# Kernel optimization log

Hardware: AMD Instinct MI355X
Metric: run time of the kernel (lower is better)

The kernel has to match this reference:

```python
import jax, jax.numpy as jnp
import numpy as np

B, T, C = 2, 2048, 1024
HS, DS = 8, 32      # short heads, short qk dim
HL, DL = 8, 128     # long heads, long qk dim
HD = 64             # value/output head dim = n_embd // n_head
WIN_S, WIN_L = 256, 1024
NEG = jnp.finfo(jnp.float32).min


def _window_mask(t, window):
    # additive mask: disallow future (i<j) and tokens older than the window
    i = jnp.arange(t)[:, None]
    j = jnp.arange(t)[None, :]
    bad = (i - j < 0) | (i - j >= window)
    return bad.astype(jnp.float32) * NEG  # [T,T]


def _attn(x, Wqk, Wv, n_h, d_qk, d_v, window):
    b, t, _ = x.shape
    qk = x @ Wqk                                      # [B,T,2*n_h*d_qk]
    q, k = jnp.split(qk, 2, axis=-1)
    q = q.reshape(b, t, n_h, d_qk).transpose(0, 2, 1, 3)  # [B,H,T,dqk]
    k = k.reshape(b, t, n_h, d_qk).transpose(0, 2, 1, 3)
    v = (x @ Wv).reshape(b, t, n_h, d_v).transpose(0, 2, 1, 3)  # [B,H,T,dv]
    scale = 1.0 / jnp.sqrt(jnp.float32(d_qk))
    scores = jnp.einsum('bhqd,bhkd->bhqk', q, k) * scale
    scores = scores + _window_mask(t, window)
    p = jax.nn.softmax(scores, axis=-1)
    return jnp.einsum('bhqk,bhkd->bhqd', p, v)        # [B,H,T,dv]


def setup_inputs() -> dict:
    key = jax.random.key(0)
    ks = jax.random.split(key, 6)
    s = 0.02
    return {
        'x': jax.random.normal(ks[0], (B, T, C), dtype=jnp.float32),
        'Wqk_short': jax.random.normal(ks[1], (C, 2 * HS * DS), dtype=jnp.float32) * s,
        'Wv_short': jax.random.normal(ks[2], (C, HS * HD), dtype=jnp.float32) * s,
        'Wqk_long': jax.random.normal(ks[3], (C, 2 * HL * DL), dtype=jnp.float32) * s,
        'Wv_long': jax.random.normal(ks[4], (C, HL * HD), dtype=jnp.float32) * s,
        'Wproj': jax.random.normal(ks[5], (C, C), dtype=jnp.float32) * s,
    }


def reference(x, Wqk_short, Wv_short, Wqk_long, Wv_long, Wproj):
    b, t, c = x.shape
    y_short = _attn(x, Wqk_short, Wv_short, HS, DS, HD, WIN_S)  # [B,HS,T,HD]
    y_long = _attn(x, Wqk_long, Wv_long, HL, DL, HD, WIN_L)     # [B,HL,T,HD]
    y = jnp.concatenate([y_short, y_long], axis=1)              # [B,H,T,HD]
    y = y.transpose(0, 2, 1, 3).reshape(b, t, c)
    return y @ Wproj
```

## Files before the change

kernel.cpp:

```cpp
#include <hip/hip_runtime.h>
#include <math.h>

#define B_    2
#define T_    2048
#define C_    1024
#define HS_   8
#define DS_   32
#define HL_   8
#define DL_   128
#define HD_   64
#define WINS_ 256
#define WINL_ 1024
#define NALL_ 3584

typedef __bf16 bf16x8 __attribute__((ext_vector_type(8)));
typedef float floatx4 __attribute__((ext_vector_type(4)));

__device__ __forceinline__ ushort f2bf(float f) {
    union { float f; unsigned u; } v; v.f = f;
    unsigned r = v.u + 0x7fff + ((v.u >> 16) & 1);
    return (ushort)(r >> 16);
}
__device__ __forceinline__ float bf2f(ushort u) {
    union { unsigned u; float f; } v; v.u = ((unsigned)u) << 16;
    return v.f;
}

__device__ __forceinline__ float dpp_bfly(float x, int ctrl_unused) { return x; }
#define DPP_STEP(x, ctrl, op)                                                \
    {                                                                        \
        float _t = __builtin_bit_cast(                                       \
            float, __builtin_amdgcn_update_dpp(                              \
                       0, __builtin_bit_cast(int, (x)), (ctrl), 0xf, 0xf,    \
                       true));                                               \
        (x) = op((x), _t);                                                   \
    }
__device__ __forceinline__ float dpp_max16(float x) {
    DPP_STEP(x, 0xB1, fmaxf);
    DPP_STEP(x, 0x4E, fmaxf);
    DPP_STEP(x, 0x141, fmaxf);
    DPP_STEP(x, 0x140, fmaxf);
    return x;
}
__device__ __forceinline__ float dpp_add16(float x) {
#define FADD_(a, b) ((a) + (b))
    DPP_STEP(x, 0xB1, FADD_);
    DPP_STEP(x, 0x4E, FADD_);
    DPP_STEP(x, 0x141, FADD_);
    DPP_STEP(x, 0x140, FADD_);
#undef FADD_
    return x;
}

__device__ __forceinline__ void gload_lds16(const void* g, void* l) {
    __builtin_amdgcn_global_load_lds(
        (const __attribute__((address_space(1))) void*)g,
        (__attribute__((address_space(3))) void*)l, 16, 0, 0);
}

__global__ __launch_bounds__(256) void prep(
    const float* __restrict__ x, ushort* __restrict__ x16,
    const float* __restrict__ Wqk_s, const float* __restrict__ Wv_s,
    const float* __restrict__ Wqk_l, const float* __restrict__ Wv_l,
    const float* __restrict__ Wproj, ushort* __restrict__ WallT,
    ushort* __restrict__ WprojT) {
    __shared__ float t[32][33];
    int bid = blockIdx.x;
    if (bid < 4096) {
        const int i = bid * 256 + threadIdx.x;
        float4 v = ((const float4*)x)[i];
        ushort4 o;
        o.x = f2bf(v.x); o.y = f2bf(v.y); o.z = f2bf(v.z); o.w = f2bf(v.w);
        ((ushort4*)x16)[i] = o;
        return;
    }
    bid -= 4096;
    const float* W; ushort* WT; int N, rowoff;
    if (bid < 512)       { W = Wqk_s; WT = WallT;  N = 512;  rowoff = 0; }
    else if (bid < 1024) { bid -= 512;  W = Wv_s;  WT = WallT;  N = 512;  rowoff = 512; }
    else if (bid < 3072) { bid -= 1024; W = Wqk_l; WT = WallT;  N = 2048; rowoff = 1024; }
    else if (bid < 3584) { bid -= 3072; W = Wv_l;  WT = WallT;  N = 512;  rowoff = 3072; }
    else                 { bid -= 3584; W = Wproj; WT = WprojT; N = 1024; rowoff = 0; }
    const int nt = N / 32;
    const int n0 = (bid % nt) * 32;
    const int k0 = (bid / nt) * 32;
    const int tx = threadIdx.x & 31;
    const int ty = threadIdx.x >> 5;
#pragma unroll
    for (int i = 0; i < 4; ++i)
        t[ty + 8 * i][tx] = W[(size_t)(k0 + ty + 8 * i) * N + n0 + tx];
    __syncthreads();
#pragma unroll
    for (int i = 0; i < 4; ++i)
        WT[(size_t)(rowoff + n0 + ty + 8 * i) * 1024 + k0 + tx] =
            f2bf(t[tx][ty + 8 * i]);
}

template <int BM, typename OT>
__global__ __launch_bounds__(256) void gemm_bf16(const ushort* __restrict__ A,
                                                 const ushort* __restrict__ BT,
                                                 OT* __restrict__ Cm,
                                                 int M, int N, int K) {
    __shared__ ushort As[BM * 32];
    __shared__ ushort Bs[128 * 32];
    constexpr int NI = BM / 32;
    const int tid = threadIdx.x;
    const int m0 = blockIdx.y * BM;
    const int n0 = blockIdx.x * 128;
    const int wave = tid >> 6;
    const int lane = tid & 63;
    const int wm = (wave >> 1) * (BM / 2);
    const int wn = (wave & 1) * 64;
    const int l15 = lane & 15;
    const int quad = lane >> 4;

    const int srow = tid >> 2;
    const int sc = (tid & 3) * 8;

    floatx4 acc[NI][4] = {};

    const ushort* Ap0 = A + (size_t)(m0 + srow) * K + sc;
    const ushort* Ap1 = A + (size_t)(m0 + (srow & 63) + 64) * K + sc;
    const ushort* Bp0 = BT + (size_t)(n0 + srow) * K + sc;
    const ushort* Bp1 = BT + (size_t)(n0 + srow + 64) * K + sc;

    ushort* AsB0 = &As[wave * 512];
    ushort* AsB1 = &As[(wave * 512 + 2048) % (BM * 32)];
    ushort* BsB0 = &Bs[wave * 512];
    ushort* BsB1 = &Bs[wave * 512 + 2048];

    for (int kt = 0; kt < K; kt += 32) {
        __syncthreads();
        gload_lds16(Ap0 + kt, AsB0);
        if constexpr (BM == 128) gload_lds16(Ap1 + kt, AsB1);
        gload_lds16(Bp0 + kt, BsB0);
        gload_lds16(Bp1 + kt, BsB1);
        __syncthreads();

        bf16x8 af[NI], bfr[4];
#pragma unroll
        for (int i = 0; i < NI; ++i)
            af[i] = *(const bf16x8*)&As[(wm + i * 16 + l15) * 32 + quad * 8];
#pragma unroll
        for (int j = 0; j < 4; ++j)
            bfr[j] = *(const bf16x8*)&Bs[(wn + j * 16 + l15) * 32 + quad * 8];
#pragma unroll
        for (int i = 0; i < NI; ++i)
#pragma unroll
            for (int j = 0; j < 4; ++j)
                acc[i][j] = __builtin_amdgcn_mfma_f32_16x16x32_bf16(
                    af[i], bfr[j], acc[i][j], 0, 0, 0);
    }

#pragma unroll
    for (int i = 0; i < NI; ++i)
#pragma unroll
        for (int j = 0; j < 4; ++j)
#pragma unroll
            for (int r = 0; r < 4; ++r) {
                const size_t idx = (size_t)(m0 + wm + i * 16 + quad * 4 + r) * N +
                                   n0 + wn + j * 16 + l15;
                if constexpr (sizeof(OT) == 2)
                    Cm[idx] = f2bf(acc[i][j][r]);
                else
                    Cm[idx] = acc[i][j][r];
            }
}

__global__ __launch_bounds__(256) void vtrans(const ushort* __restrict__ act,
                                              ushort* __restrict__ vt) {
    __shared__ ushort tile[64][72];
    const int t0 = blockIdx.x * 64;
    const int gh = blockIdx.y;
    const int b = blockIdx.z;
    const int col = (gh < 8) ? (512 + gh * 64) : (3072 + (gh - 8) * 64);
    const ushort* src = act + (size_t)(b * T_ + t0) * NALL_ + col;
    {
        const int tr = threadIdx.x >> 2;
        const int ch = threadIdx.x & 3;
        *(int4*)&tile[tr][ch * 8] =
            *(const int4*)(src + (size_t)tr * NALL_ + ch * 8);
        *(int4*)&tile[tr][(ch + 4) * 8] =
            *(const int4*)(src + (size_t)tr * NALL_ + (ch + 4) * 8);
    }
    __syncthreads();
    const int d = threadIdx.x >> 2;
    const int ts = (threadIdx.x & 3) * 16;
    ushort tmp[16];
#pragma unroll
    for (int i = 0; i < 16; ++i) tmp[i] = tile[ts + i][d];
    ushort* dst = vt + ((size_t)(b * 16 + gh) * HD_ + d) * T_ + t0 + ts;
    *(int4*)dst = *(int4*)tmp;
    *(int4*)(dst + 8) = *(int4*)(tmp + 8);
}

template <int D, int WIN, bool SPLIT>
__device__ __forceinline__ void attn_dev(
    const ushort* __restrict__ act, const ushort* __restrict__ vt,
    ushort* __restrict__ y, ushort* __restrict__ po, float* __restrict__ pm,
    float* __restrict__ pl, float scale2, int qoff, int koff, int head_off,
    int h, int gh, int b, int t0, int zs, ushort* lds) {
    constexpr int STR = D + 8;
    constexpr int PSTR = 72;
    constexpr int NKS = D / 32;
    constexpr int QCH = D / 8;
    constexpr int NKLD = (64 * QCH) / 256;

    ushort* Ks = lds;
    ushort* VTs = Ks + 64 * STR;
    ushort* Ps = VTs + 64 * PSTR;

    const int tid = threadIdx.x;
    const int wave = tid >> 6;
    const int lane = tid & 63;
    const int l15 = lane & 15;
    const int quad = lane >> 4;
    const int qmin = t0 + wave * 16;

    int k0s = t0 - WIN + 1;
    if (k0s < 0) k0s = 0;
    k0s &= ~63;

    int ks_begin = k0s, ks_last = t0;
    if (SPLIT) {
        const int nt = ((t0 - k0s) >> 6) + 1;
        const int ntlo = (nt + 1) >> 1;
        if (zs == 0) {
            ks_last = k0s + (ntlo - 1) * 64;
        } else {
            if (ntlo >= nt) {
#pragma unroll
                for (int r = 0; r < 4; ++r) {
                    const int t = qmin + quad * 4 + r;
                    const size_t ridx =
                        (((size_t)(zs * 2 + b) * 8 + h) * T_ + t);
                    if (l15 == 0) { pm[ridx] = -1e30f; pl[ridx] = 0.f; }
#pragma unroll
                    for (int j = 0; j < 4; ++j)
                        po[ridx * 64 + j * 16 + l15] = 0;
                }
                return;
            }
            ks_begin = k0s + ntlo * 64;
        }
    }

    const ushort* qbase = act + (size_t)(b * T_ + t0) * NALL_ + qoff + h * D;
    const ushort* kbase = act + (size_t)(b * T_) * NALL_ + koff + h * D;
    const ushort* vtb = vt + (size_t)((b * 16 + gh) * HD_) * T_;

    int krow[NKLD], kch[NKLD];
#pragma unroll
    for (int i = 0; i < NKLD; ++i) {
        const int idx = tid + 256 * i;
        krow[i] = idx / QCH;
        kch[i] = idx % QCH;
    }
    const int vd0 = tid >> 3, vc0 = (tid & 7) * 8;
    const int vd1 = (tid + 256) >> 3, vc1 = ((tid + 256) & 7) * 8;

    int4 kreg[NKLD], vreg0, vreg1;
#pragma unroll
    for (int i = 0; i < NKLD; ++i)
        kreg[i] = *(const int4*)(kbase + (size_t)(ks_begin + krow[i]) * NALL_ +
                                 kch[i] * 8);
    vreg0 = *(const int4*)(vtb + (size_t)vd0 * T_ + ks_begin + vc0);
    vreg1 = *(const int4*)(vtb + (size_t)vd1 * T_ + ks_begin + vc1);

    for (int idx = tid; idx < 64 * QCH; idx += 256) {
        const int row = idx / QCH;
        const int ch = idx % QCH;
        *(int4*)&Ks[row * STR + ch * 8] =
            *(const int4*)(qbase + (size_t)row * NALL_ + ch * 8);
    }
    __syncthreads();
    bf16x8 qa[NKS];
#pragma unroll
    for (int ks = 0; ks < NKS; ++ks)
        qa[ks] = *(const bf16x8*)&Ks[(wave * 16 + l15) * STR + ks * 32 + quad * 8];

    float m_i[4], l_i[4];
    floatx4 o_acc[4] = {};
#pragma unroll
    for (int r = 0; r < 4; ++r) { m_i[r] = -1e30f; l_i[r] = 0.f; }

    for (int k0 = ks_begin; k0 <= ks_last; k0 += 64) {
        __syncthreads();
#pragma unroll
        for (int i = 0; i < NKLD; ++i)
            *(int4*)&Ks[krow[i] * STR + kch[i] * 8] = kreg[i];
        *(int4*)&VTs[vd0 * PSTR + vc0] = vreg0;
        *(int4*)&VTs[vd1 * PSTR + vc1] = vreg1;
        __syncthreads();
        if (k0 + 64 <= ks_last) {
#pragma unroll
            for (int i = 0; i < NKLD; ++i)
                kreg[i] = *(const int4*)(kbase +
                                         (size_t)(k0 + 64 + krow[i]) * NALL_ +
                                         kch[i] * 8);
            vreg0 = *(const int4*)(vtb + (size_t)vd0 * T_ + k0 + 64 + vc0);
            vreg1 = *(const int4*)(vtb + (size_t)vd1 * T_ + k0 + 64 + vc1);
        }

        floatx4 s[4] = {};
#pragma unroll
        for (int ks = 0; ks < NKS; ++ks) {
#pragma unroll
            for (int j = 0; j < 4; ++j) {
                const bf16x8 bb =
                    *(const bf16x8*)&Ks[(j * 16 + l15) * STR + ks * 32 + quad * 8];
                s[j] = __builtin_amdgcn_mfma_f32_16x16x32_bf16(qa[ks], bb, s[j],
                                                               0, 0, 0);
            }
        }

        const bool full = (k0 + 63 <= qmin) && ((qmin + 15) - k0 <= WIN - 1);
        if (full) {
#pragma unroll
            for (int j = 0; j < 4; ++j)
#pragma unroll
                for (int r = 0; r < 4; ++r) s[j][r] *= scale2;
        } else {
#pragma unroll
            for (int j = 0; j < 4; ++j) {
                const int kj = k0 + j * 16 + l15;
#pragma unroll
                for (int r = 0; r < 4; ++r) {
                    const int rel = (qmin + quad * 4 + r) - kj;
                    s[j][r] = (rel < 0 || rel >= WIN) ? -1e30f : s[j][r] * scale2;
                }
            }
        }

#pragma unroll
        for (int r = 0; r < 4; ++r) {
            float rm = fmaxf(fmaxf(s[0][r], s[1][r]), fmaxf(s[2][r], s[3][r]));
            rm = dpp_max16(rm);
            const float mn = fmaxf(m_i[r], rm);
            const float a = exp2f(m_i[r] - mn);
            m_i[r] = mn;
            float sum = 0.f;
#pragma unroll
            for (int j = 0; j < 4; ++j) {
                const float e = exp2f(s[j][r] - mn);
                sum += e;
                Ps[(wave * 16 + quad * 4 + r) * PSTR + j * 16 + l15] = f2bf(e);
            }
            sum = dpp_add16(sum);
            l_i[r] = l_i[r] * a + sum;
#pragma unroll
            for (int j = 0; j < 4; ++j) o_acc[j][r] *= a;
        }

#pragma unroll
        for (int kks = 0; kks < 2; ++kks) {
            const bf16x8 pa =
                *(const bf16x8*)&Ps[(wave * 16 + l15) * PSTR + kks * 32 + quad * 8];
#pragma unroll
            for (int j = 0; j < 4; ++j) {
                const bf16x8 vb =
                    *(const bf16x8*)&VTs[(j * 16 + l15) * PSTR + kks * 32 + quad * 8];
                o_acc[j] = __builtin_amdgcn_mfma_f32_16x16x32_bf16(pa, vb, o_acc[j],
                                                                   0, 0, 0);
            }
        }
    }

    if (SPLIT) {
#pragma unroll
        for (int r = 0; r < 4; ++r) {
            const int t = qmin + quad * 4 + r;
            const size_t ridx = (((size_t)(zs * 2 + b) * 8 + h) * T_ + t);
            if (l15 == 0) { pm[ridx] = m_i[r]; pl[ridx] = l_i[r]; }
#pragma unroll
            for (int j = 0; j < 4; ++j)
                po[ridx * 64 + j * 16 + l15] = f2bf(o_acc[j][r]);
        }
    } else {
#pragma unroll
        for (int r = 0; r < 4; ++r) {
            const float inv = 1.f / l_i[r];
            ushort* yrow = y + (size_t)(b * T_ + qmin + quad * 4 + r) * C_ +
                           head_off + h * HD_;
#pragma unroll
            for (int j = 0; j < 4; ++j)
                yrow[j * 16 + l15] = f2bf(o_acc[j][r] * inv);
        }
    }
}

__global__ __launch_bounds__(256, 4) void attn_sched(
    const ushort* __restrict__ act, const ushort* __restrict__ vt,
    ushort* __restrict__ y, ushort* __restrict__ po, float* __restrict__ pm,
    float* __restrict__ pl) {
    extern __shared__ ushort smem[];
    int x = blockIdx.x;
    if (x < 1024) {
        const int zs = x & 1;
        const int b = (x >> 1) & 1;
        const int h = (x >> 2) & 7;
        const int t0 = (31 - (x >> 5)) * 64;
        attn_dev<DL_, WINL_, true>(act, vt, y, po, pm, pl,
                                   0.12752021352994164f,
                                   1024, 2048, 512, h, 8 + h, b, t0, zs, smem);
    } else {
        x -= 1024;
        const int b = x & 1;
        const int h = (x >> 1) & 7;
        const int t0 = (31 - (x >> 4)) * 64;
        attn_dev<DS_, WINS_, false>(act, vt, y, po, pm, pl,
                                    0.2550404270598833f,
                                    0, 256, 0, h, h, b, t0, 0, smem);
    }
}

__global__ __launch_bounds__(256) void combine(const ushort* __restrict__ po,
                                               const float* __restrict__ pm,
                                               const float* __restrict__ pl,
                                               ushort* __restrict__ y) {
    const int gid = blockIdx.x * 256 + threadIdx.x;
    const int row = gid >> 4;
    const int cg = (gid & 15) * 4;
    const int b = row >> 14;
    const int h = (row >> 11) & 7;
    const int t = row & 2047;

    const float m0 = pm[row], m1 = pm[32768 + row];
    const float l0 = pl[row], l1 = pl[32768 + row];
    const float m = fmaxf(m0, m1);
    const float e0 = exp2f(m0 - m);
    const float e1 = exp2f(m1 - m);
    const float inv = 1.f / (l0 * e0 + l1 * e1);

    const ushort4 o0 = *(const ushort4*)&po[(size_t)row * 64 + cg];
    const ushort4 o1 = *(const ushort4*)&po[((size_t)32768 + row) * 64 + cg];

    ushort4 r;
    r.x = f2bf((bf2f(o0.x) * e0 + bf2f(o1.x) * e1) * inv);
    r.y = f2bf((bf2f(o0.y) * e0 + bf2f(o1.y) * e1) * inv);
    r.z = f2bf((bf2f(o0.z) * e0 + bf2f(o1.z) * e1) * inv);
    r.w = f2bf((bf2f(o0.w) * e0 + bf2f(o1.w) * e1) * inv);
    *(ushort4*)&y[(size_t)(b * T_ + t) * C_ + 512 + h * 64 + cg] = r;
}

extern "C" void kernel_launch(void* const* d_in, const int* in_sizes, int n_in,
                              void* d_out, int out_size, void* d_ws,
                              size_t ws_size, hipStream_t stream) {
    const float* x         = (const float*)d_in[0];
    const float* Wqk_short = (const float*)d_in[1];
    const float* Wv_short  = (const float*)d_in[2];
    const float* Wqk_long  = (const float*)d_in[3];
    const float* Wv_long   = (const float*)d_in[4];
    const float* Wproj     = (const float*)d_in[5];
    float* out = (float*)d_out;

    const int M = B_ * T_;

    ushort* x16    = (ushort*)d_ws;
    ushort* WallT  = x16 + (size_t)M * C_;
    ushort* WprojT = WallT + (size_t)NALL_ * C_;
    ushort* yb16   = WprojT + (size_t)C_ * C_;
    ushort* act    = yb16 + (size_t)M * C_;
    ushort* vt     = act + (size_t)M * NALL_;
    ushort* po     = vt + (size_t)32 * HD_ * T_;
    float*  pm     = (float*)(po + (size_t)2 * 32768 * 64);
    float*  pl     = pm + (size_t)2 * 32768;

    dim3 blk(256);
    prep<<<dim3(8704), blk, 0, stream>>>(x, x16, Wqk_short, Wv_short, Wqk_long,
                                         Wv_long, Wproj, WallT, WprojT);

    gemm_bf16<128, ushort><<<dim3(NALL_ / 128, M / 128), blk, 0, stream>>>(
        x16, WallT, act, M, NALL_, C_);

    vtrans<<<dim3(T_ / 64, 16, B_), blk, 0, stream>>>(act, vt);

    const int attn_lds = (64 * (DL_ + 8) + 64 * 72 * 2) * 2;
    attn_sched<<<dim3(1536), blk, attn_lds, stream>>>(act, vt, yb16, po, pm, pl);

    combine<<<dim3(2048), blk, 0, stream>>>(po, pm, pl, yb16);

    gemm_bf16<64, float><<<dim3(C_ / 128, M / 64), blk, 0, stream>>>(
        yb16, WprojT, out, M, C_, C_);
}
```

Measured before the change: 220.4 us.

## Double-buffer GEMM LDS tiles and fuse V transpose into QKV GEMM epilogue

The bf16 GEMM now uses two LDS buffers, prefetching the next k-tile while the current one feeds MFMA, which halves the barriers per k-step. The QKV GEMM epilogue writes V-column tiles directly in transposed layout into the vt buffer, so the separate vtrans kernel launch and its extra read/write of V go away. The cost is doubled LDS usage, which may reduce occupancy, and transposed epilogue stores that are 8-byte and strided across T rather than coalesced.

```diff
diff --git a/kernel.cpp b/kernel.cpp
--- a/kernel.cpp
+++ b/kernel.cpp
@@ -26,7 +26,6 @@
     return v.f;
 }
 
-__device__ __forceinline__ float dpp_bfly(float x, int ctrl_unused) { return x; }
 #define DPP_STEP(x, ctrl, op)                                                \
     {                                                                        \
         float _t = __builtin_bit_cast(                                       \
@@ -96,13 +95,14 @@
             f2bf(t[tx][ty + 8 * i]);
 }
 
-template <int BM, typename OT>
+template <int BM, typename OT, bool FUSEV>
 __global__ __launch_bounds__(256) void gemm_bf16(const ushort* __restrict__ A,
                                                  const ushort* __restrict__ BT,
                                                  OT* __restrict__ Cm,
+                                                 ushort* __restrict__ VT,
                                                  int M, int N, int K) {
-    __shared__ ushort As[BM * 32];
-    __shared__ ushort Bs[128 * 32];
+    __shared__ ushort As[2][BM * 32];
+    __shared__ ushort Bs[2][128 * 32];
     constexpr int NI = BM / 32;
     const int tid = threadIdx.x;
     const int m0 = blockIdx.y * BM;
@@ -124,74 +124,83 @@
     const ushort* Bp0 = BT + (size_t)(n0 + srow) * K + sc;
     const ushort* Bp1 = BT + (size_t)(n0 + srow + 64) * K + sc;
 
-    ushort* AsB0 = &As[wave * 512];
-    ushort* AsB1 = &As[(wave * 512 + 2048) % (BM * 32)];
-    ushort* BsB0 = &Bs[wave * 512];
-    ushort* BsB1 = &Bs[wave * 512 + 2048];
-
-    for (int kt = 0; kt < K; kt += 32) {
+    const int aoff0 = wave * 512;
+    const int aoff1 = (wave * 512 + 2048) % (BM * 32);
+    const int boff0 = wave * 512;
+    const int boff1 = wave * 512 + 2048;
+
+#define STAGE(buf, kt)                                                \
+    {                                                                 \
+        gload_lds16(Ap0 + (kt), &As[buf][aoff0]);                     \
+        if constexpr (BM == 128) gload_lds16(Ap1 + (kt), &As[buf][aoff1]); \
+        gload_lds16(Bp0 + (kt), &Bs[buf][boff0]);                     \
+        gload_lds16(Bp1 + (kt), &Bs[buf][boff1]);                     \
+    }
+
+#define COMPUTE(buf)                                                       \
+    {                                                                      \
+        bf16x8 af[NI], bfr[4];                                             \
+        _Pragma("unroll") for (int i = 0; i < NI; ++i) af[i] =             \
+            *(const bf16x8*)&As[buf][(wm + i * 16 + l15) * 32 + quad * 8]; \
+        _Pragma("unroll") for (int j = 0; j < 4; ++j) bfr[j] =             \
+            *(const bf16x8*)&Bs[buf][(wn + j * 16 + l15) * 32 + quad * 8]; \
+        _Pragma("unroll") for (int i = 0; i < NI; ++i)                     \
+            _Pragma("unroll") for (int j = 0; j < 4; ++j) acc[i][j] =      \
+                __builtin_amdgcn_mfma_f32_16x16x32_bf16(af[i], bfr[j],     \
+                                                        acc[i][j], 0, 0, 0); \
+    }
+
+    STAGE(0, 0);
+    __syncthreads();
+    for (int kt = 0; kt < K; kt += 64) {
+        STAGE(1, kt + 32);
+        COMPUTE(0);
         __syncthreads();
-        gload_lds16(Ap0 + kt, AsB0);
-        if constexpr (BM == 128) gload_lds16(Ap1 + kt, AsB1);
-        gload_lds16(Bp0 + kt, BsB0);
-        gload_lds16(Bp1 + kt, BsB1);
+        if (kt + 64 < K) STAGE(0, kt + 64);
+        COMPUTE(1);
         __syncthreads();
-
-        bf16x8 af[NI], bfr[4];
+    }
+#undef STAGE
+#undef COMPUTE
+
+    bool vtile = false;
+    if constexpr (FUSEV)
+        vtile = (n0 >= 512 && n0 < 1024) || (n0 >= 3072);
+
+    if (FUSEV && vtile) {
+#pragma unroll
+        for (int i = 0; i < NI; ++i) {
+            const int m = m0 + wm + i * 16 + quad * 4;
+            const int bb = m >> 11;
+            const int t = m & 2047;
+#pragma unroll
+            for (int j = 0; j < 4; ++j) {
+                const int col = n0 + wn + j * 16 + l15;
+                const int vcol = (col < 1024) ? (col - 512) : (col - 2560);
+                ushort4 val;
+                val.x = f2bf(acc[i][j][0]);
+                val.y = f2bf(acc[i][j][1]);
+                val.z = f2bf(acc[i][j][2]);
+                val.w = f2bf(acc[i][j][3]);
+                *(ushort4*)&VT[((size_t)(bb * 1024 + vcol)) * T_ + t] = val;
+            }
+        }
+    } else {
 #pragma unroll
         for (int i = 0; i < NI; ++i)
-            af[i] = *(const bf16x8*)&As[(wm + i * 16 + l15) * 32 + quad * 8];
-#pragma unroll
-        for (int j = 0; j < 4; ++j)
-            bfr[j] = *(const bf16x8*)&Bs[(wn + j * 16 + l15) * 32 + quad * 8];
-#pragma unroll
-        for (int i = 0; i < NI; ++i)
 #pragma unroll
             for (int j = 0; j < 4; ++j)
-                acc[i][j] = __builtin_amdgcn_mfma_f32_16x16x32_bf16(
-                    af[i], bfr[j], acc[i][j], 0, 0, 0);
-    }
-
-#pragma unroll
-    for (int i = 0; i < NI; ++i)
-#pragma unroll
-        for (int j = 0; j < 4; ++j)
-#pragma unroll
-            for (int r = 0; r < 4; ++r) {
-                const size_t idx = (size_t)(m0 + wm + i * 16 + quad * 4 + r) * N +
-                                   n0 + wn + j * 16 + l15;
-                if constexpr (sizeof(OT) == 2)
-                    Cm[idx] = f2bf(acc[i][j][r]);
-                else
-                    Cm[idx] = acc[i][j][r];
-            }
-}
-
-__global__ __launch_bounds__(256) void vtrans(const ushort* __restrict__ act,
-                                              ushort* __restrict__ vt) {
-    __shared__ ushort tile[64][72];
-    const int t0 = blockIdx.x * 64;
-    const int gh = blockIdx.y;
-    const int b = blockIdx.z;
-    const int col = (gh < 8) ? (512 + gh * 64) : (3072 + (gh - 8) * 64);
-    const ushort* src = act + (size_t)(b * T_ + t0) * NALL_ + col;
-    {
-        const int tr = threadIdx.x >> 2;
-        const int ch = threadIdx.x & 3;
-        *(int4*)&tile[tr][ch * 8] =
-            *(const int4*)(src + (size_t)tr * NALL_ + ch * 8);
-        *(int4*)&tile[tr][(ch + 4) * 8] =
-            *(const int4*)(src + (size_t)tr * NALL_ + (ch + 4) * 8);
-    }
-    __syncthreads();
-    const int d = threadIdx.x >> 2;
-    const int ts = (threadIdx.x & 3) * 16;
-    ushort tmp[16];
-#pragma unroll
-    for (int i = 0; i < 16; ++i) tmp[i] = tile[ts + i][d];
-    ushort* dst = vt + ((size_t)(b * 16 + gh) * HD_ + d) * T_ + t0 + ts;
-    *(int4*)dst = *(int4*)tmp;
-    *(int4*)(dst + 8) = *(int4*)(tmp + 8);
+#pragma unroll
+                for (int r = 0; r < 4; ++r) {
+                    const size_t idx =
+                        (size_t)(m0 + wm + i * 16 + quad * 4 + r) * N + n0 +
+                        wn + j * 16 + l15;
+                    if constexpr (sizeof(OT) == 2)
+                        Cm[idx] = f2bf(acc[i][j][r]);
+                    else
+                        Cm[idx] = acc[i][j][r];
+                }
+    }
 }
 
 template <int D, int WIN, bool SPLIT>
@@ -470,16 +479,14 @@
     prep<<<dim3(8704), blk, 0, stream>>>(x, x16, Wqk_short, Wv_short, Wqk_long,
                                          Wv_long, Wproj, WallT, WprojT);
 
-    gemm_bf16<128, ushort><<<dim3(NALL_ / 128, M / 128), blk, 0, stream>>>(
-        x16, WallT, act, M, NALL_, C_);
-
-    vtrans<<<dim3(T_ / 64, 16, B_), blk, 0, stream>>>(act, vt);
+    gemm_bf16<128, ushort, true><<<dim3(NALL_ / 128, M / 128), blk, 0, stream>>>(
+        x16, WallT, act, vt, M, NALL_, C_);
 
     const int attn_lds = (64 * (DL_ + 8) + 64 * 72 * 2) * 2;
     attn_sched<<<dim3(1536), blk, attn_lds, stream>>>(act, vt, yb16, po, pm, pl);
 
     combine<<<dim3(2048), blk, 0, stream>>>(po, pm, pl, yb16);
 
-    gemm_bf16<64, float><<<dim3(C_ / 128, M / 64), blk, 0, stream>>>(
-        yb16, WprojT, out, M, C_, C_);
-}
+    gemm_bf16<64, float, false><<<dim3(C_ / 128, M / 64), blk, 0, stream>>>(
+        yb16, WprojT, out, nullptr, M, C_, C_);
+}
```

Result: no change. 219.7 us (-0.3%).
